# Performance work log

Measured on AMD Instinct MI355X. Metric: run time of the kernel, lower is better.

Reference implementation:

```python
import jax, jax.numpy as jnp
import numpy as np


def _lstm_cell(x, h, c, Wih, Whh, b):
    # PyTorch gate order: i, f, g, o
    g = x @ Wih.T + h @ Whh.T + b
    i, f, gg, o = jnp.split(g, 4, axis=-1)
    c2 = jax.nn.sigmoid(f) * c + jax.nn.sigmoid(i) * jnp.tanh(gg)
    h2 = jax.nn.sigmoid(o) * jnp.tanh(c2)
    return h2, c2


def _lstm_seq(x_tbd, h0, c0, Wih, Whh, b):
    # x_tbd: [T, B, D] -> outputs [T, B, H]
    def step(carry, xt):
        h, c = carry
        h2, c2 = _lstm_cell(xt, h, c, Wih, Whh, b)
        return (h2, c2), h2
    _, ys = jax.lax.scan(step, (h0, c0), x_tbd)
    return ys


def setup_inputs() -> dict:
    key = jax.random.key(0)
    ks = jax.random.split(key, 20)
    H, D, A, HOR, NQ = 256, 32, 128, 24, 3
    B, T = 256, 512
    s = 0.1
    inp = {
        'x':      jax.random.normal(ks[0], (B, T, D), jnp.float32),
        'e_Wih0': jax.random.normal(ks[1], (4 * H, D), jnp.float32) * s,
        'e_Whh0': jax.random.normal(ks[2], (4 * H, H), jnp.float32) * s,
        'e_b0':   jax.random.normal(ks[3], (4 * H,), jnp.float32) * s,
        'e_Wih1': jax.random.normal(ks[4], (4 * H, H), jnp.float32) * s,
        'e_Whh1': jax.random.normal(ks[5], (4 * H, H), jnp.float32) * s,
        'e_b1':   jax.random.normal(ks[6], (4 * H,), jnp.float32) * s,
        'd_Wih0': jax.random.normal(ks[7], (4 * H, 1), jnp.float32) * s,
        'd_Whh0': jax.random.normal(ks[8], (4 * H, H), jnp.float32) * s,
        'd_b0':   jax.random.normal(ks[9], (4 * H,), jnp.float32) * s,
        'd_Wih1': jax.random.normal(ks[10], (4 * H, H), jnp.float32) * s,
        'd_Whh1': jax.random.normal(ks[11], (4 * H, H), jnp.float32) * s,
        'd_b1':   jax.random.normal(ks[12], (4 * H,), jnp.float32) * s,
        'aW':     jax.random.normal(ks[13], (H, A), jnp.float32) * s,
        'aV':     jax.random.normal(ks[14], (A,), jnp.float32) * s,
        'qW':     jax.random.normal(ks[15], (NQ, HOR, H), jnp.float32) * s,
        'qb':     jax.random.normal(ks[16], (NQ, HOR), jnp.float32) * s,
    }
    return inp


def reference(x, e_Wih0, e_Whh0, e_b0, e_Wih1, e_Whh1, e_b1,
              d_Wih0, d_Whh0, d_b0, d_Wih1, d_Whh1, d_b1,
              aW, aV, qW, qb):
    B = x.shape[0]
    H = e_Whh0.shape[1]
    horizon = qW.shape[1]

    # ---- encoder: 2-layer LSTM over time ----
    xt = jnp.swapaxes(x, 0, 1)                      # [T, B, D]
    z = jnp.zeros((B, H), x.dtype)
    h1 = _lstm_seq(xt, z, z, e_Wih0, e_Whh0, e_b0)  # [T, B, H]
    h2 = _lstm_seq(h1, z, z, e_Wih1, e_Whh1, e_b1)  # [T, B, H]
    enc = jnp.swapaxes(h2, 0, 1)                    # [B, T, H]

    # ---- attention over encoder outputs ----
    energy = jnp.tanh(enc @ aW) @ aV                # [B, T]
    w = jax.nn.softmax(energy, axis=1)
    context = jnp.einsum('bt,bth->bh', w, enc)      # [B, H]

    inp0 = x[:, -1, -1:]                            # [B, 1]

    def dstep(carry, _):
        h0_, c0_, h1_, c1_, dinp = carry
        h0n, c0n = _lstm_cell(dinp, h0_, c0_, d_Wih0, d_Whh0, d_b0)
        h1n, c1n = _lstm_cell(h0n, h1_, c1_, d_Wih1, d_Whh1, d_b1)
        return (h0n, c0n, h1n, c1n, h1n[:, :1]), h1n

    _, douts = jax.lax.scan(dstep, (context, context, context, context, inp0),
                            None, length=horizon)   # [horizon, B, H]

    # ---- quantile heads on last decoder step ----
    last = douts[-1]                                # [B, H]
    preds = jnp.einsum('bh,qoh->bqo', last, qW) + qb  # [B, n_quantiles, horizon]
    return preds
```

## Files before the change

### kernel.cpp

```cpp
#include <hip/hip_runtime.h>

typedef unsigned short u16;
typedef unsigned int u32;
typedef unsigned long long u64;
typedef short v8s __attribute__((ext_vector_type(8)));
typedef float v4f __attribute__((ext_vector_type(4)));


__device__ __forceinline__ float bf2f(u16 u) { union { u32 u; float f; } c; c.u = ((u32)u) << 16; return c.f; }
__device__ __forceinline__ u16 f2bf(float f) {
  union { float f; u32 u; } c; c.f = f;
  u32 r = c.u + 0x7FFFu + ((c.u >> 16) & 1u);
  return (u16)(r >> 16);
}
__device__ __forceinline__ float sigf(float x) { return 1.f / (1.f + __expf(-x)); }
__device__ __forceinline__ float tanhfast(float x) {
  x = fminf(15.f, fmaxf(-15.f, x));
  float e = __expf(2.f * x);
  return (e - 1.f) / (e + 1.f);
}
__device__ __forceinline__ float ldIn(const void* p, size_t i, int isbf) {
  return isbf ? bf2f(((const u16*)p)[i]) : ((const float*)p)[i];
}
__device__ __forceinline__ v8s ld8hi(const void* p, size_t e, int isbf) {
  if (isbf) return *(const v8s*)((const u16*)p + e);
  const float* f = (const float*)p + e;
  v8s r;
#pragma unroll
  for (int j = 0; j < 8; ++j) r[j] = (short)f2bf(f[j]);
  return r;
}
__device__ __forceinline__ void ld8split(const void* p, size_t e, int isbf, v8s& hi, v8s& lo) {
  if (isbf) {
    hi = *(const v8s*)((const u16*)p + e);
    lo = v8s{0, 0, 0, 0, 0, 0, 0, 0};
  } else {
    const float* f = (const float*)p + e;
#pragma unroll
    for (int j = 0; j < 8; ++j) {
      u16 h = f2bf(f[j]);
      hi[j] = (short)h;
      lo[j] = (short)f2bf(f[j] - bf2f(h));
    }
  }
}
#define MFMA(a, b, c) __builtin_amdgcn_mfma_f32_16x16x32_bf16(a, b, c, 0, 0, 0)

__device__ __forceinline__ u64 aload64(const u64* p) {
  return __hip_atomic_load(p, __ATOMIC_RELAXED, __HIP_MEMORY_SCOPE_AGENT);
}
__device__ __forceinline__ void astore64(u64* p, u64 v) {
  __hip_atomic_store(p, v, __ATOMIC_RELAXED, __HIP_MEMORY_SCOPE_AGENT);
}

__device__ __forceinline__ void stage_dec(u16* dhi, u16* dlo, const u64* src,
                                          int tid, u32 tag) {
  u64 v[16];
#pragma unroll
  for (int i = 0; i < 16; ++i) v[i] = aload64(src + i * 256 + tid);
  bool all;
  do {
    all = true;
#pragma unroll
    for (int i = 0; i < 16; ++i) {
      if ((u32)(v[i] >> 32) != tag) { all = false; v[i] = aload64(src + i * 256 + tid); }
    }
  } while (!all);
#pragma unroll
  for (int i = 0; i < 16; ++i) {
    int idx = i * 256 + tid;
    int row = idx >> 8, col = idx & 255;
    dhi[row * 264 + col] = (u16)v[i];
    dlo[row * 264 + col] = (u16)(v[i] >> 16);
  }
}
__device__ __forceinline__ void stage_f32(u16* dhi, u16* dlo, const float* src, int tid) {
#pragma unroll
  for (int i = 0; i < 8; ++i) {
    int e = i * 512 + tid * 2;
    int row = e >> 8, jc = e & 255;
    float f0 = src[row * 256 + jc], f1 = src[row * 256 + jc + 1];
    u16 h0 = f2bf(f0), h1 = f2bf(f1);
    u16 l0 = f2bf(f0 - bf2f(h0)), l1 = f2bf(f1 - bf2f(h1));
    ((u32*)(dhi + row * 264))[jc >> 1] = (u32)h0 | ((u32)h1 << 16);
    ((u32*)(dlo + row * 264))[jc >> 1] = (u32)l0 | ((u32)l1 << 16);
  }
}

__global__ void sniff_kernel(const u16* __restrict__ w, int* __restrict__ flag) {
  __shared__ int cnt;
  if (threadIdx.x == 0) cnt = 0;
  __syncthreads();
  int ok = 0;
  for (int i = threadIdx.x; i < 1024; i += 256) {
    u16 u = w[2 * i];
    int e = (u >> 7) & 0xFF;
    ok += (u == 0 || (e >= 97 && e <= 140)) ? 1 : 0;
  }
  atomicAdd(&cnt, ok);
  __syncthreads();
  if (threadIdx.x == 0) *flag = (cnt >= 768) ? 1 : 0;
}

__global__ __launch_bounds__(256, 1) void enc_kernel(
    const void* __restrict__ x,
    const void* __restrict__ eWih0, const void* __restrict__ eWhh0, const void* __restrict__ eb0,
    const void* __restrict__ eWih1, const void* __restrict__ eWhh1, const void* __restrict__ eb1,
    const void* __restrict__ aW, const void* __restrict__ aV,
    u64* __restrict__ C,
    float* __restrict__ ctx, const int* __restrict__ flagp) {
  __shared__ __align__(16) u16 h0s[16 * 264], h1s[16 * 264];
  __shared__ float gb0[16 * 64], gb1[16 * 64];
  __shared__ float eP[16 * 132];

  const int isbf = *flagp;
  const int tid = threadIdx.x, blk = blockIdx.x;
  const int grp = blk & 15, gs = blk >> 4;
  const int lane = tid & 63, wv = tid >> 6;
  const int ln = lane & 15, lq = lane >> 4;

  v8s W0F[9], W1F[16], AWF[16];
  {
    const int gw = wv * 256 + gs * 16 + ln;
    const int kq = lq * 8;
    W0F[0] = ld8hi(eWih0, (size_t)gw * 32 + kq, isbf);
#pragma unroll
    for (int kt = 0; kt < 8; ++kt) {
      W0F[kt + 1] = ld8hi(eWhh0, (size_t)gw * 256 + kt * 32 + kq, isbf);
      W1F[kt]     = ld8hi(eWhh1, (size_t)gw * 256 + kt * 32 + kq, isbf);
      W1F[kt + 8] = ld8hi(eWih1, (size_t)gw * 256 + kt * 32 + kq, isbf);
    }
#pragma unroll
    for (int kt = 0; kt < 8; ++kt)
#pragma unroll
      for (int j2 = 0; j2 < 2; ++j2) {
        v8s f;
        int ac = (2 * wv + j2) * 16 + ln;
#pragma unroll
        for (int j = 0; j < 8; ++j)
          f[j] = (short)f2bf(ldIn(aW, (size_t)(kt * 32 + kq + j) * 128 + ac, isbf));
        AWF[kt * 2 + j2] = f;
      }
  }

  const int urow = tid >> 4, uu = tid & 15;
  float bg0[4], bg1[4], aVr[8];
#pragma unroll
  for (int g = 0; g < 4; ++g) {
    bg0[g] = ldIn(eb0, g * 256 + gs * 16 + uu, isbf);
    bg1[g] = ldIn(eb1, g * 256 + gs * 16 + uu, isbf);
  }
#pragma unroll
  for (int j = 0; j < 8; ++j) aVr[j] = ldIn(aV, (size_t)(uu + 16 * j), isbf);

  const int gRowU = grp * 16 + urow;
  const int gUnit = gs * 16 + uu;
  const int aRow = grp * 16 + ln;
  const u32 stOff = (u32)(grp * 4096 + gs * 256 + urow * 16 + uu);

  float c0 = 0.f, c1 = 0.f;
  float mS = -3e38f, lS = 0.f, ctxA = 0.f;

  v8s xh_c, xl_c;
  ld8split(x, ((size_t)aRow * 512) * 32 + lq * 8, isbf, xh_c, xl_c);
  v8s a0r[8];

#pragma unroll 1
  for (int t = 0; t < 514; ++t) {
    const int rPar = (t + 1) & 1, wPar = t & 1;
    const u32 tag = (u32)(u16)t;
    {
      const u64* src = C + (size_t)rPar * 65536 + grp * 4096;
      u64 v[16];
#pragma unroll
      for (int i = 0; i < 16; ++i) v[i] = aload64(src + i * 256 + tid);
      bool all;
      do {
        all = true;
#pragma unroll
        for (int i = 0; i < 16; ++i) {
          u64 w = v[i];
          if (!((((w >> 16) & 0xFFFFull) == tag) && ((w >> 48) == tag))) {
            all = false;
            v[i] = aload64(src + i * 256 + tid);
          }
        }
      } while (!all);
#pragma unroll
      for (int i = 0; i < 16; ++i) {
        u64 w = v[i];
        h0s[urow * 264 + i * 16 + uu] = (u16)w;
        h1s[urow * 264 + i * 16 + uu] = (u16)(w >> 32);
      }
    }
    __syncthreads();

#pragma unroll
    for (int kt = 0; kt < 8; ++kt)
      a0r[kt] = *(const v8s*)(h0s + ln * 264 + kt * 32 + lq * 8);
    if (t < 512) {
      v4f acc0 = {0, 0, 0, 0};
      acc0 = MFMA(xh_c, W0F[0], acc0);
      if (!isbf) acc0 = MFMA(xl_c, W0F[0], acc0);
#pragma unroll
      for (int kt = 0; kt < 8; ++kt) acc0 = MFMA(a0r[kt], W0F[kt + 1], acc0);
#pragma unroll
      for (int r = 0; r < 4; ++r) gb0[(lq * 4 + r) * 64 + ln * 4 + wv] = acc0[r];
    }
    {
      v4f acc1 = {0, 0, 0, 0}, accA0 = {0, 0, 0, 0}, accA1 = {0, 0, 0, 0};
#pragma unroll
      for (int kt = 0; kt < 8; ++kt) {
        v8s a1 = *(const v8s*)(h1s + ln * 264 + kt * 32 + lq * 8);
        acc1 = MFMA(a0r[kt], W1F[kt + 8], acc1);
        acc1 = MFMA(a1, W1F[kt], acc1);
        accA0 = MFMA(a1, AWF[kt * 2], accA0);
        accA1 = MFMA(a1, AWF[kt * 2 + 1], accA1);
      }
#pragma unroll
      for (int r = 0; r < 4; ++r) {
        gb1[(lq * 4 + r) * 64 + ln * 4 + wv] = acc1[r];
        eP[(lq * 4 + r) * 132 + (2 * wv) * 16 + ln] = accA0[r];
        eP[(lq * 4 + r) * 132 + (2 * wv + 1) * 16 + ln] = accA1[r];
      }
    }
    v8s xh_n, xl_n;
    {
      int tn = (t + 1 < 512) ? t + 1 : 511;
      ld8split(x, ((size_t)aRow * 512 + tn) * 32 + lq * 8, isbf, xh_n, xl_n);
    }
    float h1v = bf2f(h1s[urow * 264 + gUnit]);
    __syncthreads();

    const u32 tagS = (u32)(u16)(t + 1) << 16;
    if (t <= 512) {
      u32 w0 = tagS, w1 = tagS;
      if (t < 512) {
        const float* g0 = gb0 + (urow * 16 + uu) * 4;
        float gi = g0[0] + bg0[0], gf = g0[1] + bg0[1], gg = g0[2] + bg0[2], go = g0[3] + bg0[3];
        c0 = sigf(gf) * c0 + sigf(gi) * tanhfast(gg);
        float h = sigf(go) * tanhfast(c0);
        w0 |= (u32)f2bf(h);
      }
      if (t >= 1) {
        const float* g1 = gb1 + (urow * 16 + uu) * 4;
        float gi = g1[0] + bg1[0], gf = g1[1] + bg1[1], gg = g1[2] + bg1[2], go = g1[3] + bg1[3];
        c1 = sigf(gf) * c1 + sigf(gi) * tanhfast(gg);
        float h = sigf(go) * tanhfast(c1);
        w1 |= (u32)f2bf(h);
      }
      astore64(C + (size_t)wPar * 65536 + stOff, (u64)w0 | ((u64)w1 << 32));
    }
    if (t >= 2) {
      float e = 0.f;
#pragma unroll
      for (int j = 0; j < 8; ++j)
        e += tanhfast(eP[urow * 132 + uu + 16 * j]) * aVr[j];
      e += __shfl_xor(e, 1);
      e += __shfl_xor(e, 2);
      e += __shfl_xor(e, 4);
      e += __shfl_xor(e, 8);
      float nm = fmaxf(mS, e);
      float al = __expf(mS - nm), p = __expf(e - nm);
      lS = lS * al + p;
      ctxA = ctxA * al + p * h1v;
      mS = nm;
    }
    xh_c = xh_n; xl_c = xl_n;
  }
  ctx[(size_t)gRowU * 256 + gUnit] = ctxA / lS;
}

__global__ __launch_bounds__(256, 1) void dec_kernel(
    const void* __restrict__ x,
    const void* __restrict__ dWih0, const void* __restrict__ dWhh0, const void* __restrict__ db0,
    const void* __restrict__ dWih1, const void* __restrict__ dWhh1, const void* __restrict__ db1,
    const void* __restrict__ qW, const void* __restrict__ qb,
    const float* __restrict__ ctx,
    u64* __restrict__ H0d, u64* __restrict__ H1d, u64* __restrict__ dinpG,
    void* __restrict__ out, const int* __restrict__ flagp) {
  __shared__ u16 sAhi[16 * 264], sAlo[16 * 264], sBhi[16 * 264], sBlo[16 * 264];
  __shared__ float gb[16 * 64];
  __shared__ float dinpS[16];

  const int isbf = *flagp;
  const int tid = threadIdx.x, blk = blockIdx.x;
  const int grp = blk & 15, gs = blk >> 4;
  const int lane = tid & 63, wv = tid >> 6;
  const int ln = lane & 15, lq = lane >> 4;

  v8s W0F[8], W1F[16];
  {
    const int gw = wv * 256 + gs * 16 + ln;
    const int kq = lq * 8;
#pragma unroll
    for (int kt = 0; kt < 8; ++kt) {
      W0F[kt]     = ld8hi(dWhh0, (size_t)gw * 256 + kt * 32 + kq, isbf);
      W1F[kt]     = ld8hi(dWhh1, (size_t)gw * 256 + kt * 32 + kq, isbf);
      W1F[kt + 8] = ld8hi(dWih1, (size_t)gw * 256 + kt * 32 + kq, isbf);
    }
  }
  const int urow = tid >> 4, uu = tid & 15;
  float bg0[4], bg1[4], w0v[4];
#pragma unroll
  for (int g = 0; g < 4; ++g) {
    bg0[g] = ldIn(db0, g * 256 + gs * 16 + uu, isbf);
    bg1[g] = ldIn(db1, g * 256 + gs * 16 + uu, isbf);
    w0v[g] = ldIn(dWih0, g * 256 + gs * 16 + uu, isbf);
  }
  const int gRowU = grp * 16 + urow;
  const int gUnit = gs * 16 + uu;

  float c0 = ctx[(size_t)gRowU * 256 + gUnit];
  float c1 = c0;

#pragma unroll 1
  for (int t = 0; t < 24; ++t) {
    const int pPrev = (t + 1) & 1, pCur = t & 1;
    if (t == 0) {
      stage_f32(sAhi, sAlo, ctx + (size_t)grp * 16 * 256, tid);
      if (tid < 16)
        dinpS[tid] = ldIn(x, ((size_t)(grp * 16 + tid) * 512 + 511) * 32 + 31, isbf);
    } else {
      stage_dec(sAhi, sAlo, H0d + (size_t)pPrev * 65536 + grp * 4096, tid, (u32)(2 * t - 1));
      if (tid < 16) {
        u64 w;
        do { w = aload64(dinpG + pPrev * 256 + grp * 16 + tid); } while ((u32)(w >> 32) != (u32)(2 * t));
        dinpS[tid] = __uint_as_float((u32)w);
      }
    }
    __syncthreads();
    v4f acc = {0, 0, 0, 0};
#pragma unroll
    for (int kt = 0; kt < 8; ++kt) {
      const int off = ln * 264 + kt * 32 + lq * 8;
      acc = MFMA(*(const v8s*)(sAhi + off), W0F[kt], acc);
      acc = MFMA(*(const v8s*)(sAlo + off), W0F[kt], acc);
    }
    {
      const int bR = lq * 4;
#pragma unroll
      for (int r = 0; r < 4; ++r) gb[(bR + r) * 64 + ln * 4 + wv] = acc[r];
    }
    float di = dinpS[urow];
    __syncthreads();
    {
      const float* g0 = gb + (urow * 16 + uu) * 4;
      float gi = g0[0] + bg0[0] + di * w0v[0];
      float gf = g0[1] + bg0[1] + di * w0v[1];
      float gg = g0[2] + bg0[2] + di * w0v[2];
      float go = g0[3] + bg0[3] + di * w0v[3];
      c0 = sigf(gf) * c0 + sigf(gi) * tanhfast(gg);
      float h = sigf(go) * tanhfast(c0);
      u16 hh = f2bf(h); u16 hl = f2bf(h - bf2f(hh));
      astore64(H0d + (size_t)pCur * 65536 + gRowU * 256 + gUnit,
               (u64)hh | ((u64)hl << 16) | ((u64)(u32)(2 * t + 1) << 32));
    }
    if (t == 0) stage_f32(sBhi, sBlo, ctx + (size_t)grp * 16 * 256, tid);
    else stage_dec(sBhi, sBlo, H1d + (size_t)pPrev * 65536 + grp * 4096, tid, (u32)(2 * t));
    stage_dec(sAhi, sAlo, H0d + (size_t)pCur * 65536 + grp * 4096, tid, (u32)(2 * t + 1));
    __syncthreads();
    v4f a1 = {0, 0, 0, 0};
#pragma unroll
    for (int kt = 0; kt < 8; ++kt) {
      const int off = ln * 264 + kt * 32 + lq * 8;
      a1 = MFMA(*(const v8s*)(sBhi + off), W1F[kt], a1);
      a1 = MFMA(*(const v8s*)(sBlo + off), W1F[kt], a1);
      a1 = MFMA(*(const v8s*)(sAhi + off), W1F[kt + 8], a1);
      a1 = MFMA(*(const v8s*)(sAlo + off), W1F[kt + 8], a1);
    }
    {
      const int bR = lq * 4;
#pragma unroll
      for (int r = 0; r < 4; ++r) gb[(bR + r) * 64 + ln * 4 + wv] = a1[r];
    }
    __syncthreads();
    {
      const float* g1 = gb + (urow * 16 + uu) * 4;
      float gi = g1[0] + bg1[0], gf = g1[1] + bg1[1], gg = g1[2] + bg1[2], go = g1[3] + bg1[3];
      c1 = sigf(gf) * c1 + sigf(gi) * tanhfast(gg);
      float h = sigf(go) * tanhfast(c1);
      u16 hh = f2bf(h); u16 hl = f2bf(h - bf2f(hh));
      astore64(H1d + (size_t)pCur * 65536 + gRowU * 256 + gUnit,
               (u64)hh | ((u64)hl << 16) | ((u64)(u32)(2 * t + 2) << 32));
      if (gUnit == 0)
        astore64(dinpG + pCur * 256 + gRowU,
                 (u64)__float_as_uint(h) | ((u64)(u32)(2 * t + 2) << 32));
    }
  }
  stage_dec(sAhi, sAlo, H1d + (size_t)65536 + grp * 4096, tid, 48u);
  __syncthreads();
  if (gs < 12 && tid < 96) {
    int r = tid / 6, p = tid % 6;
    int qo = gs * 6 + p, row = grp * 16 + r;
    float s = ldIn(qb, qo, isbf);
    for (int h = 0; h < 256; ++h)
      s += (bf2f(sAhi[r * 264 + h]) + bf2f(sAlo[r * 264 + h])) * ldIn(qW, (size_t)qo * 256 + h, isbf);
    if (isbf) ((u16*)out)[row * 72 + qo] = f2bf(s);
    else      ((float*)out)[row * 72 + qo] = s;
  }
}

extern "C" void kernel_launch(void* const* d_in, const int* in_sizes, int n_in,
                              void* d_out, int out_size, void* d_ws, size_t ws_size,
                              hipStream_t stream) {
  const void* x     = d_in[0];
  const void* eWih0 = d_in[1];
  const void* eWhh0 = d_in[2];
  const void* eb0   = d_in[3];
  const void* eWih1 = d_in[4];
  const void* eWhh1 = d_in[5];
  const void* eb1   = d_in[6];
  const void* dWih0 = d_in[7];
  const void* dWhh0 = d_in[8];
  const void* db0   = d_in[9];
  const void* dWih1 = d_in[10];
  const void* dWhh1 = d_in[11];
  const void* db1   = d_in[12];
  const void* aW    = d_in[13];
  const void* aV    = d_in[14];
  const void* qW    = d_in[15];
  const void* qb    = d_in[16];

  char* wsb = (char*)d_ws;
  u64*   C     = (u64*)(wsb + 0);
  u64*   H0d   = (u64*)(wsb + 1048576);
  u64*   H1d   = (u64*)(wsb + 2097152);
  u64*   dinpG = (u64*)(wsb + 3145728);
  int*   flag  = (int*)(wsb + 3149824);
  float* ctx   = (float*)(wsb + 3150080);

  hipMemsetAsync(wsb, 0, 3149824, stream);

  sniff_kernel<<<1, 256, 0, stream>>>((const u16*)eWhh0, flag);
  enc_kernel<<<256, 256, 0, stream>>>(x, eWih0, eWhh0, eb0, eWih1, eWhh1, eb1,
                                      aW, aV, C, ctx, flag);
  dec_kernel<<<256, 256, 0, stream>>>(x, dWih0, dWhh0, db0, dWih1, dWhh1, db1,
                                      qW, qb, ctx, H0d, H1d, dinpG,
                                      d_out, flag);
}
```

Measured before the change: 2.064 ms.

## Move attention MFMAs off critical path and swizzle LDS to cut bank conflicts

Moves the attention-energy MFMAs and the next x load to after the h/c store to global, so the cross-block state exchange for the next step is published sooner and other blocks wait less. Adds an XOR swizzle on the h0s/h1s LDS layout and changes the gate buffers to a padded gate-major layout, both to reduce LDS bank conflicts. Also skips the exchange poll on the final step. The cost is an extra __syncthreads per timestep and more registers held for a1r.

```diff
diff --git a/kernel.cpp b/kernel.cpp
--- a/kernel.cpp
+++ b/kernel.cpp
@@ -110,7 +110,7 @@
     u64* __restrict__ C,
     float* __restrict__ ctx, const int* __restrict__ flagp) {
   __shared__ __align__(16) u16 h0s[16 * 264], h1s[16 * 264];
-  __shared__ float gb0[16 * 64], gb1[16 * 64];
+  __shared__ float gb0[4 * 280], gb1[4 * 280];
   __shared__ float eP[16 * 132];
 
   const int isbf = *flagp;
@@ -163,13 +163,13 @@
 
   v8s xh_c, xl_c;
   ld8split(x, ((size_t)aRow * 512) * 32 + lq * 8, isbf, xh_c, xl_c);
-  v8s a0r[8];
+  v8s a0r[8], a1r[8];
 
 #pragma unroll 1
   for (int t = 0; t < 514; ++t) {
     const int rPar = (t + 1) & 1, wPar = t & 1;
     const u32 tag = (u32)(u16)t;
-    {
+    if (t <= 512) {
       const u64* src = C + (size_t)rPar * 65536 + grp * 4096;
       u64 v[16];
 #pragma unroll
@@ -189,15 +189,21 @@
 #pragma unroll
       for (int i = 0; i < 16; ++i) {
         u64 w = v[i];
-        h0s[urow * 264 + i * 16 + uu] = (u16)w;
-        h1s[urow * 264 + i * 16 + uu] = (u16)(w >> 32);
-      }
-    }
-    __syncthreads();
-
-#pragma unroll
-    for (int kt = 0; kt < 8; ++kt)
-      a0r[kt] = *(const v8s*)(h0s + ln * 264 + kt * 32 + lq * 8);
+        int sw = ((i ^ urow) << 4) + uu;
+        h0s[urow * 264 + sw] = (u16)w;
+        h1s[urow * 264 + sw] = (u16)(w >> 32);
+      }
+    }
+    __syncthreads();
+
+#pragma unroll
+    for (int kt = 0; kt < 8; ++kt) {
+      int b = kt * 2 + (lq >> 1);
+      int off = ln * 264 + (((b ^ ln) << 4)) + (lq & 1) * 8;
+      a0r[kt] = *(const v8s*)(h0s + off);
+      a1r[kt] = *(const v8s*)(h1s + off);
+    }
+    float h1v = bf2f(h1s[urow * 264 + (((gs ^ urow) << 4)) + uu]);
     if (t < 512) {
       v4f acc0 = {0, 0, 0, 0};
       acc0 = MFMA(xh_c, W0F[0], acc0);
@@ -205,52 +211,60 @@
 #pragma unroll
       for (int kt = 0; kt < 8; ++kt) acc0 = MFMA(a0r[kt], W0F[kt + 1], acc0);
 #pragma unroll
-      for (int r = 0; r < 4; ++r) gb0[(lq * 4 + r) * 64 + ln * 4 + wv] = acc0[r];
-    }
-    {
-      v4f acc1 = {0, 0, 0, 0}, accA0 = {0, 0, 0, 0}, accA1 = {0, 0, 0, 0};
+      for (int r = 0; r < 4; ++r) gb0[wv * 280 + (lq * 4 + r) * 17 + ln] = acc0[r];
+    }
+    {
+      v4f acc1 = {0, 0, 0, 0};
 #pragma unroll
       for (int kt = 0; kt < 8; ++kt) {
-        v8s a1 = *(const v8s*)(h1s + ln * 264 + kt * 32 + lq * 8);
         acc1 = MFMA(a0r[kt], W1F[kt + 8], acc1);
-        acc1 = MFMA(a1, W1F[kt], acc1);
-        accA0 = MFMA(a1, AWF[kt * 2], accA0);
-        accA1 = MFMA(a1, AWF[kt * 2 + 1], accA1);
-      }
-#pragma unroll
-      for (int r = 0; r < 4; ++r) {
-        gb1[(lq * 4 + r) * 64 + ln * 4 + wv] = acc1[r];
-        eP[(lq * 4 + r) * 132 + (2 * wv) * 16 + ln] = accA0[r];
-        eP[(lq * 4 + r) * 132 + (2 * wv + 1) * 16 + ln] = accA1[r];
-      }
-    }
-    v8s xh_n, xl_n;
-    {
-      int tn = (t + 1 < 512) ? t + 1 : 511;
-      ld8split(x, ((size_t)aRow * 512 + tn) * 32 + lq * 8, isbf, xh_n, xl_n);
-    }
-    float h1v = bf2f(h1s[urow * 264 + gUnit]);
+        acc1 = MFMA(a1r[kt], W1F[kt], acc1);
+      }
+#pragma unroll
+      for (int r = 0; r < 4; ++r) gb1[wv * 280 + (lq * 4 + r) * 17 + ln] = acc1[r];
+    }
     __syncthreads();
 
     const u32 tagS = (u32)(u16)(t + 1) << 16;
     if (t <= 512) {
       u32 w0 = tagS, w1 = tagS;
+      const int o = urow * 17 + uu;
       if (t < 512) {
-        const float* g0 = gb0 + (urow * 16 + uu) * 4;
-        float gi = g0[0] + bg0[0], gf = g0[1] + bg0[1], gg = g0[2] + bg0[2], go = g0[3] + bg0[3];
+        float gi = gb0[o] + bg0[0], gf = gb0[280 + o] + bg0[1];
+        float gg = gb0[560 + o] + bg0[2], go = gb0[840 + o] + bg0[3];
         c0 = sigf(gf) * c0 + sigf(gi) * tanhfast(gg);
         float h = sigf(go) * tanhfast(c0);
         w0 |= (u32)f2bf(h);
       }
       if (t >= 1) {
-        const float* g1 = gb1 + (urow * 16 + uu) * 4;
-        float gi = g1[0] + bg1[0], gf = g1[1] + bg1[1], gg = g1[2] + bg1[2], go = g1[3] + bg1[3];
+        float gi = gb1[o] + bg1[0], gf = gb1[280 + o] + bg1[1];
+        float gg = gb1[560 + o] + bg1[2], go = gb1[840 + o] + bg1[3];
         c1 = sigf(gf) * c1 + sigf(gi) * tanhfast(gg);
         float h = sigf(go) * tanhfast(c1);
         w1 |= (u32)f2bf(h);
       }
       astore64(C + (size_t)wPar * 65536 + stOff, (u64)w0 | ((u64)w1 << 32));
     }
+
+    {
+      v4f accA0 = {0, 0, 0, 0}, accA1 = {0, 0, 0, 0};
+#pragma unroll
+      for (int kt = 0; kt < 8; ++kt) {
+        accA0 = MFMA(a1r[kt], AWF[kt * 2], accA0);
+        accA1 = MFMA(a1r[kt], AWF[kt * 2 + 1], accA1);
+      }
+#pragma unroll
+      for (int r = 0; r < 4; ++r) {
+        eP[(lq * 4 + r) * 132 + (2 * wv) * 16 + ln] = accA0[r];
+        eP[(lq * 4 + r) * 132 + (2 * wv + 1) * 16 + ln] = accA1[r];
+      }
+    }
+    v8s xh_n, xl_n;
+    {
+      int tn = (t + 1 < 512) ? t + 1 : 511;
+      ld8split(x, ((size_t)aRow * 512 + tn) * 32 + lq * 8, isbf, xh_n, xl_n);
+    }
+    __syncthreads();
     if (t >= 2) {
       float e = 0.f;
 #pragma unroll
```

Result: slower. 2.231 ms (+8.1%).

## Move attention energy MFMAs off the recurrent critical path with double-buffered scratch

Applied to the files above, without the earlier changes.

The attention-energy MFMAs are taken out of the recurrent section between the two barriers and run after the state publish. They write into a double-buffered eP array and are consumed one step later, with an epilogue after the loop. The per-gate MFMA chains are also split into two independent accumulators to shorten dependency latency. This shortens the serial step that other blocks wait on, at the cost of extra shared memory, more registers (a1r) and extra epilogue logic.

```diff
diff --git a/kernel.cpp b/kernel.cpp
--- a/kernel.cpp
+++ b/kernel.cpp
@@ -111,7 +111,7 @@
     float* __restrict__ ctx, const int* __restrict__ flagp) {
   __shared__ __align__(16) u16 h0s[16 * 264], h1s[16 * 264];
   __shared__ float gb0[16 * 64], gb1[16 * 64];
-  __shared__ float eP[16 * 132];
+  __shared__ float eP[2][16 * 132];
 
   const int isbf = *flagp;
   const int tid = threadIdx.x, blk = blockIdx.x;
@@ -160,10 +160,11 @@
 
   float c0 = 0.f, c1 = 0.f;
   float mS = -3e38f, lS = 0.f, ctxA = 0.f;
+  float h1v = 0.f;
 
   v8s xh_c, xl_c;
   ld8split(x, ((size_t)aRow * 512) * 32 + lq * 8, isbf, xh_c, xl_c);
-  v8s a0r[8];
+  v8s a0r[8], a1r[8];
 
 #pragma unroll 1
   for (int t = 0; t < 514; ++t) {
@@ -196,40 +197,32 @@
     __syncthreads();
 
 #pragma unroll
-    for (int kt = 0; kt < 8; ++kt)
-      a0r[kt] = *(const v8s*)(h0s + ln * 264 + kt * 32 + lq * 8);
+    for (int kt = 0; kt < 8; ++kt) {
+      const int off = ln * 264 + kt * 32 + lq * 8;
+      a0r[kt] = *(const v8s*)(h0s + off);
+      a1r[kt] = *(const v8s*)(h1s + off);
+    }
     if (t < 512) {
-      v4f acc0 = {0, 0, 0, 0};
-      acc0 = MFMA(xh_c, W0F[0], acc0);
-      if (!isbf) acc0 = MFMA(xl_c, W0F[0], acc0);
-#pragma unroll
-      for (int kt = 0; kt < 8; ++kt) acc0 = MFMA(a0r[kt], W0F[kt + 1], acc0);
-#pragma unroll
-      for (int r = 0; r < 4; ++r) gb0[(lq * 4 + r) * 64 + ln * 4 + wv] = acc0[r];
-    }
-    {
-      v4f acc1 = {0, 0, 0, 0}, accA0 = {0, 0, 0, 0}, accA1 = {0, 0, 0, 0};
+      v4f A = {0, 0, 0, 0}, B = {0, 0, 0, 0};
+      A = MFMA(xh_c, W0F[0], A);
+      if (!isbf) A = MFMA(xl_c, W0F[0], A);
+#pragma unroll
+      for (int kt = 0; kt < 4; ++kt) A = MFMA(a0r[kt], W0F[kt + 1], A);
+#pragma unroll
+      for (int kt = 4; kt < 8; ++kt) B = MFMA(a0r[kt], W0F[kt + 1], B);
+#pragma unroll
+      for (int r = 0; r < 4; ++r) gb0[(lq * 4 + r) * 64 + ln * 4 + wv] = A[r] + B[r];
+    }
+    {
+      v4f A = {0, 0, 0, 0}, B = {0, 0, 0, 0};
 #pragma unroll
       for (int kt = 0; kt < 8; ++kt) {
-        v8s a1 = *(const v8s*)(h1s + ln * 264 + kt * 32 + lq * 8);
-        acc1 = MFMA(a0r[kt], W1F[kt + 8], acc1);
-        acc1 = MFMA(a1, W1F[kt], acc1);
-        accA0 = MFMA(a1, AWF[kt * 2], accA0);
-        accA1 = MFMA(a1, AWF[kt * 2 + 1], accA1);
-      }
-#pragma unroll
-      for (int r = 0; r < 4; ++r) {
-        gb1[(lq * 4 + r) * 64 + ln * 4 + wv] = acc1[r];
-        eP[(lq * 4 + r) * 132 + (2 * wv) * 16 + ln] = accA0[r];
-        eP[(lq * 4 + r) * 132 + (2 * wv + 1) * 16 + ln] = accA1[r];
-      }
-    }
-    v8s xh_n, xl_n;
-    {
-      int tn = (t + 1 < 512) ? t + 1 : 511;
-      ld8split(x, ((size_t)aRow * 512 + tn) * 32 + lq * 8, isbf, xh_n, xl_n);
-    }
-    float h1v = bf2f(h1s[urow * 264 + gUnit]);
+        A = MFMA(a0r[kt], W1F[kt + 8], A);
+        B = MFMA(a1r[kt], W1F[kt], B);
+      }
+#pragma unroll
+      for (int r = 0; r < 4; ++r) gb1[(lq * 4 + r) * 64 + ln * 4 + wv] = A[r] + B[r];
+    }
     __syncthreads();
 
     const u32 tagS = (u32)(u16)(t + 1) << 16;
@@ -251,11 +244,13 @@
       }
       astore64(C + (size_t)wPar * 65536 + stOff, (u64)w0 | ((u64)w1 << 32));
     }
-    if (t >= 2) {
+
+    if (t >= 3) {
+      const float* ep = eP[(t + 1) & 1];
       float e = 0.f;
 #pragma unroll
       for (int j = 0; j < 8; ++j)
-        e += tanhfast(eP[urow * 132 + uu + 16 * j]) * aVr[j];
+        e += tanhfast(ep[urow * 132 + uu + 16 * j]) * aVr[j];
       e += __shfl_xor(e, 1);
       e += __shfl_xor(e, 2);
       e += __shfl_xor(e, 4);
@@ -266,7 +261,42 @@
       ctxA = ctxA * al + p * h1v;
       mS = nm;
     }
-    xh_c = xh_n; xl_c = xl_n;
+    if (t >= 2) {
+      v4f A = {0, 0, 0, 0}, B = {0, 0, 0, 0};
+#pragma unroll
+      for (int kt = 0; kt < 8; ++kt) {
+        A = MFMA(a1r[kt], AWF[kt * 2], A);
+        B = MFMA(a1r[kt], AWF[kt * 2 + 1], B);
+      }
+      float* ep = eP[t & 1];
+#pragma unroll
+      for (int r = 0; r < 4; ++r) {
+        ep[(lq * 4 + r) * 132 + (2 * wv) * 16 + ln] = A[r];
+        ep[(lq * 4 + r) * 132 + (2 * wv + 1) * 16 + ln] = B[r];
+      }
+      h1v = bf2f(h1s[urow * 264 + gUnit]);
+    }
+    {
+      int tn = (t + 1 < 512) ? t + 1 : 511;
+      ld8split(x, ((size_t)aRow * 512 + tn) * 32 + lq * 8, isbf, xh_c, xl_c);
+    }
+  }
+  __syncthreads();
+  {
+    const float* ep = eP[1];
+    float e = 0.f;
+#pragma unroll
+    for (int j = 0; j < 8; ++j)
+      e += tanhfast(ep[urow * 132 + uu + 16 * j]) * aVr[j];
+    e += __shfl_xor(e, 1);
+    e += __shfl_xor(e, 2);
+    e += __shfl_xor(e, 4);
+    e += __shfl_xor(e, 8);
+    float nm = fmaxf(mS, e);
+    float al = __expf(mS - nm), p = __expf(e - nm);
+    lS = lS * al + p;
+    ctxA = ctxA * al + p * h1v;
+    mS = nm;
   }
   ctx[(size_t)gRowU * 256 + gUnit] = ctxA / lS;
 }
```

Result: no change. 2.053 ms (-0.5%).
